# Kernel tuning notes

Hardware: AMD Instinct MI355X
Metric: run time of the kernel (lower is better)

## Reference

```python
import jax, jax.numpy as jnp
import numpy as np

EPS = 1e-12  # F.normalize default eps (denominator = max(norm, eps))


def setup_inputs() -> dict:
    key = jax.random.key(0)
    ks = jax.random.split(key, 8)
    B, FIN, H, W = 4, 256, 64, 64
    N_MEM, SQ = 64, 16           # sqrt_fin = fin**0.5
    POS_CH = 2                    # PosEncoding concatenates one coord channel per dim
    CIN = FIN + POS_CH
    QK = N_MEM * SQ               # 1024
    # PosEncoding buffer: normalized coordinate grid in [-1, 1], shape [2, H, W]
    ys = jnp.linspace(-1.0, 1.0, H, dtype=jnp.float32)
    xs = jnp.linspace(-1.0, 1.0, W, dtype=jnp.float32)
    gy, gx = jnp.meshgrid(ys, xs, indexing='ij')
    pos = jnp.stack([gy, gx], axis=0)
    s = 0.02
    return {
        'x':    jax.random.normal(ks[0], (B, FIN, H, W), jnp.float32),
        'pos':  pos,
        'wq':   jax.random.normal(ks[1], (QK, CIN), jnp.float32) * s,
        'bq':   jnp.zeros((QK,), jnp.float32),
        'wk':   jax.random.normal(ks[2], (QK, CIN), jnp.float32) * s,
        'bk':   jnp.zeros((QK,), jnp.float32),
        'v':    jax.random.normal(ks[3], (N_MEM, FIN), jnp.float32) * s,
        'wout': jax.random.normal(ks[4], (FIN, FIN), jnp.float32) * s,
        'bout': jnp.zeros((FIN,), jnp.float32),
    }


def reference(x, pos, wq, bq, wk, bk, v, wout, bout):
    B, C, H, W = x.shape
    S = H * W
    n_mem, fin = v.shape
    sq = wq.shape[0] // n_mem
    # PosEncoding: concat coordinate channels
    posb = jnp.broadcast_to(pos[None], (B,) + pos.shape)
    xp = jnp.concatenate([x, posb], axis=1).reshape(B, C + pos.shape[0], S)
    # 1x1 conv projections (channel GEMMs)
    q = jnp.einsum('oc,bcs->bos', wq, xp) + bq[None, :, None]  # [B, n_mem*sq, S]
    k = jnp.einsum('oc,bcs->bos', wk, xp) + bk[None, :, None]
    q = q.reshape(B, n_mem, sq, S).transpose(0, 3, 1, 2)  # [B,S,m,sq]
    k = k.reshape(B, n_mem, sq, S).transpose(0, 3, 2, 1)  # [B,S,sq,m]
    # F.normalize: q over last dim (sqrt_fin), k over dim=1 (sqrt_fin)
    qn = q / jnp.maximum(jnp.linalg.norm(q, axis=-1, keepdims=True), EPS)
    kn = k / jnp.maximum(jnp.linalg.norm(k, axis=2, keepdims=True), EPS)
    # attn[b,s,m,n] = qn . kn ; dropout is identity in eval mode.
    # mean over memory slots m commutes with (attn @ v), so fuse:
    attn_mean = jnp.einsum('bsk,bskn->bsn', qn.mean(axis=2), kn)  # [B,S,n_mem]
    mem = attn_mean @ v                                            # [B,S,fin]
    mem = mem.transpose(0, 2, 1).reshape(B, fin, H, W)
    out = jnp.einsum('of,bfhw->bohw', wout, mem) + bout[None, :, None, None]
    return x + out
```

## Files before the change

kernel.cpp:

```cpp
#include <hip/hip_runtime.h>
#include <stdint.h>

#define EPSN 1e-12f

typedef float f32x16 __attribute__((ext_vector_type(16)));
typedef float f32x4 __attribute__((ext_vector_type(4)));
typedef __bf16 bf16x8 __attribute__((ext_vector_type(8)));

__device__ __forceinline__ unsigned short f2bf(float f) {
  union { float f; unsigned int u; } v; v.f = f;
  unsigned int u = v.u + 0x7FFFu + ((v.u >> 16) & 1u);
  return (unsigned short)(u >> 16);
}

#define NKS 17
#define WQF_OFF 0
#define WKF_OFF (32 * NKS * 64 * 8)
#define WVP_OFF (2 * 32 * NKS * 64 * 8)

__global__ __launch_bounds__(256) void prep_kernel(
    const float* __restrict__ wq, const float* __restrict__ bq,
    const float* __restrict__ wk, const float* __restrict__ bk,
    const float* __restrict__ v, const float* __restrict__ wout,
    unsigned short* __restrict__ wsp) {
  int bid = blockIdx.x;
  if (bid < 512) {
    int isK = bid >= 256;
    int ob = (bid & 255) * 4;
    const float* w = isK ? wk : wq;
    const float* bb = isK ? bk : bq;
    unsigned short* dst = wsp + (isK ? WKF_OFF : WQF_OFF);
    for (int i = threadIdx.x; i < 4 * 129; i += 256) {
      int r = i / 129, q = i - r * 129;
      int o = ob + r, k = q * 2;
      float2 w2 = *(const float2*)(w + o * 258 + k);
      int g = o >> 5, col = o & 31;
      int ks = k >> 4, hi = (k >> 3) & 1, j = k & 7;
      uint32_t pk = (uint32_t)f2bf(w2.x) | ((uint32_t)f2bf(w2.y) << 16);
      *(uint32_t*)(dst + (((g * NKS + ks) * 64 + hi * 32 + col) << 3) + j) = pk;
    }
    for (int i = threadIdx.x; i < 4 * 14; i += 256) {
      int r = i / 14, kk = 258 + (i - r * 14);
      int o = ob + r;
      int g = o >> 5, col = o & 31;
      int ks = kk >> 4, hi = (kk >> 3) & 1, j = kk & 7;
      dst[(((g * NKS + ks) * 64 + hi * 32 + col) << 3) + j] =
          (kk == 258) ? f2bf(bb[o]) : (unsigned short)0;
    }
  } else {
    int idx = (bid - 512) * 256 + threadIdx.x;
    int fc = idx & 15, m = (idx >> 4) & 63, o = idx >> 10;
    const f32x4* wo = (const f32x4*)(wout + o * 256 + fc * 16);
    const f32x4* vm = (const f32x4*)(v + m * 256 + fc * 16);
    float s = 0.f;
#pragma unroll
    for (int f = 0; f < 4; ++f) {
      f32x4 a = wo[f], bvv = vm[f];
      s += a[0]*bvv[0] + a[1]*bvv[1] + a[2]*bvv[2] + a[3]*bvv[3];
    }
    s += __shfl_xor(s, 1, 64);
    s += __shfl_xor(s, 2, 64);
    s += __shfl_xor(s, 4, 64);
    s += __shfl_xor(s, 8, 64);
    if (fc == 0) wsp[WVP_OFF + o * 64 + m] = f2bf(s);
  }
}

#define KP 296
#define QS 66
#define AT 72

__global__ __launch_bounds__(1024, 4) void fused_kernel(
    const float* __restrict__ x, const float* __restrict__ pos,
    const unsigned short* __restrict__ wsp, const float* __restrict__ bout,
    float* __restrict__ out) {
  __shared__ __align__(16) unsigned short xp[64 * KP];
  __shared__ __align__(16) float qbarL[16 * QS];
  __shared__ __align__(16) unsigned short attnM[64 * AT];
  __shared__ float boutL[256];

  const int tid = threadIdx.x;
  const int lane = tid & 63;
  const int wid = __builtin_amdgcn_readfirstlane(tid >> 6);
  const int px = lane & 31, q2 = lane >> 5;
  const int P0 = blockIdx.x * 64;
  const int b = P0 >> 12, s0 = P0 & 4095;

  const int wtoff = (2 * wid) * NKS * 512 + lane * 8;
  const unsigned short* wqf = wsp + WQF_OFF + wtoff;
  const unsigned short* wkf = wsp + WKF_OFF + wtoff;

  bf16x8 A0 = *(const bf16x8*)(wqf);
  bf16x8 A1 = *(const bf16x8*)(wqf + NKS * 512);

  uint32_t* xp32 = (uint32_t*)xp;
  {
    const float* xrow = x + b * 256 * 4096 + s0;
    float v0[8], v1[8];
#pragma unroll
    for (int it = 0; it < 8; ++it) {
      int item = tid + it * 1024;
      int pp = item & 63, dcol = item >> 6;
      v0[it] = xrow[(2 * dcol) * 4096 + pp];
      v1[it] = xrow[(2 * dcol + 1) * 4096 + pp];
    }
#pragma unroll
    for (int it = 0; it < 8; ++it) {
      int item = tid + it * 1024;
      int pp = item & 63, dcol = item >> 6;
      xp32[pp * 148 + dcol] =
          (uint32_t)f2bf(v0[it]) | ((uint32_t)f2bf(v1[it]) << 16);
    }
    if (tid < 512) {
      int pp = tid & 63, dcol = 128 + (tid >> 6);
      float t0 = 0.f, t1 = 0.f;
      if (dcol == 128) { t0 = pos[s0 + pp]; t1 = pos[4096 + s0 + pp]; }
      else if (dcol == 129) { t0 = 1.0f; }
      xp32[pp * 148 + dcol] = (uint32_t)f2bf(t0) | ((uint32_t)f2bf(t1) << 16);
    }
  }
  if (tid < 256) boutL[tid] = bout[tid];
  for (int i = tid; i < 16 * QS; i += 1024) qbarL[i] = 0.f;
  __syncthreads();

#define PHASE(WB, AI0, AI1) do {                                          \
    bf16x8 _A0 = (AI0), _A1 = (AI1);                                      \
    _Pragma("unroll")                                                     \
    for (int ks = 0; ks < NKS; ++ks) {                                    \
      bf16x8 _N0 = _A0, _N1 = _A1;                                        \
      if (ks + 1 < NKS) {                                                 \
        _N0 = *(const bf16x8*)((WB) + (ks + 1) * 512);                    \
        _N1 = *(const bf16x8*)((WB) + NKS * 512 + (ks + 1) * 512);        \
      }                                                                   \
      bf16x8 _b0 = *(const bf16x8*)&xp[px * KP + ks * 16 + q2 * 8];       \
      bf16x8 _b1 = *(const bf16x8*)&xp[(32 + px) * KP + ks * 16 + q2 * 8];\
      acc00 = __builtin_amdgcn_mfma_f32_32x32x16_bf16(_A0, _b0, acc00, 0, 0, 0); \
      acc01 = __builtin_amdgcn_mfma_f32_32x32x16_bf16(_A0, _b1, acc01, 0, 0, 0); \
      acc10 = __builtin_amdgcn_mfma_f32_32x32x16_bf16(_A1, _b0, acc10, 0, 0, 0); \
      acc11 = __builtin_amdgcn_mfma_f32_32x32x16_bf16(_A1, _b1, acc11, 0, 0, 0); \
      _A0 = _N0; _A1 = _N1;                                               \
    }                                                                     \
  } while (0)

  f32x16 acc00 = (f32x16)0.f, acc01 = (f32x16)0.f,
         acc10 = (f32x16)0.f, acc11 = (f32x16)0.f;
  PHASE(wqf, A0, A1);

  bf16x8 K0 = *(const bf16x8*)(wkf);
  bf16x8 K1 = *(const bf16x8*)(wkf + NKS * 512);

  {
    float qsum[2][8];
#pragma unroll
    for (int nt = 0; nt < 2; ++nt)
#pragma unroll
      for (int r = 0; r < 8; ++r) qsum[nt][r] = 0.f;
#pragma unroll
    for (int ot = 0; ot < 2; ++ot) {
#pragma unroll
      for (int nt = 0; nt < 2; ++nt) {
        const f32x16 a = ot ? (nt ? acc11 : acc10) : (nt ? acc01 : acc00);
        float s20 = 0.f, s21 = 0.f;
#pragma unroll
        for (int r = 0; r < 8; ++r) {
          s20 = fmaf(a[r], a[r], s20);
          s21 = fmaf(a[r + 8], a[r + 8], s21);
        }
        s20 += __shfl_xor(s20, 32, 64);
        s21 += __shfl_xor(s21, 32, 64);
        float i0 = 1.0f / fmaxf(sqrtf(s20), EPSN);
        float i1 = 1.0f / fmaxf(sqrtf(s21), EPSN);
#pragma unroll
        for (int r = 0; r < 8; ++r) qsum[nt][r] += a[r] * i0 + a[r + 8] * i1;
      }
    }
#pragma unroll
    for (int nt = 0; nt < 2; ++nt)
#pragma unroll
      for (int r = 0; r < 8; ++r) {
        int j = (r & 3) + ((r >> 2) << 3) + (q2 << 2);
        atomicAdd(&qbarL[j * QS + nt * 32 + px], qsum[nt][r] * (1.0f / 64.0f));
      }
  }
  __syncthreads();

  acc00 = (f32x16)0.f; acc01 = (f32x16)0.f;
  acc10 = (f32x16)0.f; acc11 = (f32x16)0.f;
  PHASE(wkf, K0, K1);

  {
    float qb[2][8];
#pragma unroll
    for (int nt = 0; nt < 2; ++nt)
#pragma unroll
      for (int r = 0; r < 8; ++r) {
        int j = (r & 3) + ((r >> 2) << 3) + (q2 << 2);
        qb[nt][r] = qbarL[j * QS + nt * 32 + px];
      }
#pragma unroll
    for (int ot = 0; ot < 2; ++ot) {
#pragma unroll
      for (int nt = 0; nt < 2; ++nt) {
        const f32x16 a = ot ? (nt ? acc11 : acc10) : (nt ? acc01 : acc00);
        float s20 = 0.f, s21 = 0.f, sp0 = 0.f, sp1 = 0.f;
#pragma unroll
        for (int r = 0; r < 8; ++r) {
          s20 = fmaf(a[r], a[r], s20);         sp0 = fmaf(qb[nt][r], a[r], sp0);
          s21 = fmaf(a[r + 8], a[r + 8], s21); sp1 = fmaf(qb[nt][r], a[r + 8], sp1);
        }
        s20 += __shfl_xor(s20, 32, 64);
        s21 += __shfl_xor(s21, 32, 64);
        sp0 += __shfl_xor(sp0, 32, 64);
        sp1 += __shfl_xor(sp1, 32, 64);
        if (q2 == 0) {
          int m0 = wid * 4 + ot * 2;
          attnM[(nt * 32 + px) * AT + m0]     = f2bf(sp0 / fmaxf(sqrtf(s20), EPSN));
          attnM[(nt * 32 + px) * AT + m0 + 1] = f2bf(sp1 / fmaxf(sqrtf(s21), EPSN));
        }
      }
    }
  }
  __syncthreads();

  {
    const int otile = wid >> 1, pxt = wid & 1;
    f32x16 e = (f32x16)0.f;
    const unsigned short* wv = wsp + WVP_OFF + (otile * 32 + px) * 64 + q2 * 8;
    const unsigned short* ab = &attnM[(pxt * 32 + px) * AT + q2 * 8];
#pragma unroll
    for (int ks = 0; ks < 4; ++ks) {
      bf16x8 av = *(const bf16x8*)(wv + ks * 16);
      bf16x8 bv = *(const bf16x8*)(ab + ks * 16);
      e = __builtin_amdgcn_mfma_f32_32x32x16_bf16(av, bv, e, 0, 0, 0);
    }
#pragma unroll
    for (int r = 0; r < 16; ++r) {
      const int o = otile * 32 + (r & 3) + ((r >> 2) << 3) + (q2 << 2);
      const int p = pxt * 32 + px;
      const int gi = (b * 256 + o) * 4096 + s0 + p;
      out[gi] = x[gi] + boutL[o] + e[r];
    }
  }
#undef PHASE
}

extern "C" void kernel_launch(void* const* d_in, const int* in_sizes, int n_in,
                              void* d_out, int out_size, void* d_ws, size_t ws_size,
                              hipStream_t stream) {
  const float* x    = (const float*)d_in[0];
  const float* pos  = (const float*)d_in[1];
  const float* wq   = (const float*)d_in[2];
  const float* bq   = (const float*)d_in[3];
  const float* wk   = (const float*)d_in[4];
  const float* bk   = (const float*)d_in[5];
  const float* v    = (const float*)d_in[6];
  const float* wout = (const float*)d_in[7];
  const float* bout = (const float*)d_in[8];
  float* out = (float*)d_out;
  unsigned short* wsp = (unsigned short*)d_ws;

  hipLaunchKernelGGL(prep_kernel, dim3(1536), dim3(256), 0, stream,
                     wq, bq, wk, bk, v, wout, wsp);
  hipLaunchKernelGGL(fused_kernel, dim3(256), dim3(1024), 0, stream,
                     x, pos, wsp, bout, out);
}
```

Baseline: 134.4 us.

## Halve pixel tile per block to 32 and double grid to 512 blocks

```diff
diff --git a/kernel.cpp b/kernel.cpp
--- a/kernel.cpp
+++ b/kernel.cpp
@@ -66,53 +66,51 @@
   }
 }
 
+#define PXB 32
 #define KP 296
-#define QS 66
-#define AT 72
-
-__global__ __launch_bounds__(1024, 4) void fused_kernel(
+#define QS 34
+#define AT 76
+
+__global__ __launch_bounds__(1024, 8) void fused_kernel(
     const float* __restrict__ x, const float* __restrict__ pos,
     const unsigned short* __restrict__ wsp, const float* __restrict__ bout,
     float* __restrict__ out) {
-  __shared__ __align__(16) unsigned short xp[64 * KP];
+  __shared__ __align__(16) unsigned short xp[PXB * KP];
   __shared__ __align__(16) float qbarL[16 * QS];
-  __shared__ __align__(16) unsigned short attnM[64 * AT];
+  __shared__ __align__(16) unsigned short attnM[PXB * AT];
   __shared__ float boutL[256];
 
   const int tid = threadIdx.x;
   const int lane = tid & 63;
   const int wid = __builtin_amdgcn_readfirstlane(tid >> 6);
   const int px = lane & 31, q2 = lane >> 5;
-  const int P0 = blockIdx.x * 64;
+  const int P0 = blockIdx.x * PXB;
   const int b = P0 >> 12, s0 = P0 & 4095;
 
   const int wtoff = (2 * wid) * NKS * 512 + lane * 8;
   const unsigned short* wqf = wsp + WQF_OFF + wtoff;
   const unsigned short* wkf = wsp + WKF_OFF + wtoff;
 
-  bf16x8 A0 = *(const bf16x8*)(wqf);
-  bf16x8 A1 = *(const bf16x8*)(wqf + NKS * 512);
-
   uint32_t* xp32 = (uint32_t*)xp;
   {
     const float* xrow = x + b * 256 * 4096 + s0;
-    float v0[8], v1[8];
-#pragma unroll
-    for (int it = 0; it < 8; ++it) {
+    float v0[4], v1[4];
+#pragma unroll
+    for (int it = 0; it < 4; ++it) {
       int item = tid + it * 1024;
-      int pp = item & 63, dcol = item >> 6;
+      int pp = item & 31, dcol = item >> 5;
       v0[it] = xrow[(2 * dcol) * 4096 + pp];
       v1[it] = xrow[(2 * dcol + 1) * 4096 + pp];
     }
 #pragma unroll
-    for (int it = 0; it < 8; ++it) {
+    for (int it = 0; it < 4; ++it) {
       int item = tid + it * 1024;
-      int pp = item & 63, dcol = item >> 6;
+      int pp = item & 31, dcol = item >> 5;
       xp32[pp * 148 + dcol] =
           (uint32_t)f2bf(v0[it]) | ((uint32_t)f2bf(v1[it]) << 16);
     }
-    if (tid < 512) {
-      int pp = tid & 63, dcol = 128 + (tid >> 6);
+    if (tid < 256) {
+      int pp = tid & 31, dcol = 128 + (tid >> 5);
       float t0 = 0.f, t1 = 0.f;
       if (dcol == 128) { t0 = pos[s0 + pp]; t1 = pos[4096 + s0 + pp]; }
       else if (dcol == 129) { t0 = 1.0f; }
@@ -123,110 +121,85 @@
   for (int i = tid; i < 16 * QS; i += 1024) qbarL[i] = 0.f;
   __syncthreads();
 
-#define PHASE(WB, AI0, AI1) do {                                          \
-    bf16x8 _A0 = (AI0), _A1 = (AI1);                                      \
+#define PHASE(WB) do {                                                    \
     _Pragma("unroll")                                                     \
     for (int ks = 0; ks < NKS; ++ks) {                                    \
-      bf16x8 _N0 = _A0, _N1 = _A1;                                        \
-      if (ks + 1 < NKS) {                                                 \
-        _N0 = *(const bf16x8*)((WB) + (ks + 1) * 512);                    \
-        _N1 = *(const bf16x8*)((WB) + NKS * 512 + (ks + 1) * 512);        \
-      }                                                                   \
+      bf16x8 _A0 = *(const bf16x8*)((WB) + ks * 512);                     \
+      bf16x8 _A1 = *(const bf16x8*)((WB) + NKS * 512 + ks * 512);         \
       bf16x8 _b0 = *(const bf16x8*)&xp[px * KP + ks * 16 + q2 * 8];       \
-      bf16x8 _b1 = *(const bf16x8*)&xp[(32 + px) * KP + ks * 16 + q2 * 8];\
-      acc00 = __builtin_amdgcn_mfma_f32_32x32x16_bf16(_A0, _b0, acc00, 0, 0, 0); \
-      acc01 = __builtin_amdgcn_mfma_f32_32x32x16_bf16(_A0, _b1, acc01, 0, 0, 0); \
-      acc10 = __builtin_amdgcn_mfma_f32_32x32x16_bf16(_A1, _b0, acc10, 0, 0, 0); \
-      acc11 = __builtin_amdgcn_mfma_f32_32x32x16_bf16(_A1, _b1, acc11, 0, 0, 0); \
-      _A0 = _N0; _A1 = _N1;                                               \
+      acc0 = __builtin_amdgcn_mfma_f32_32x32x16_bf16(_A0, _b0, acc0, 0, 0, 0); \
+      acc1 = __builtin_amdgcn_mfma_f32_32x32x16_bf16(_A1, _b0, acc1, 0, 0, 0); \
     }                                                                     \
   } while (0)
 
-  f32x16 acc00 = (f32x16)0.f, acc01 = (f32x16)0.f,
-         acc10 = (f32x16)0.f, acc11 = (f32x16)0.f;
-  PHASE(wqf, A0, A1);
-
-  bf16x8 K0 = *(const bf16x8*)(wkf);
-  bf16x8 K1 = *(const bf16x8*)(wkf + NKS * 512);
+  f32x16 acc0 = (f32x16)0.f, acc1 = (f32x16)0.f;
+  PHASE(wqf);
 
   {
-    float qsum[2][8];
-#pragma unroll
-    for (int nt = 0; nt < 2; ++nt)
-#pragma unroll
-      for (int r = 0; r < 8; ++r) qsum[nt][r] = 0.f;
+    float qsum[8];
+#pragma unroll
+    for (int r = 0; r < 8; ++r) qsum[r] = 0.f;
 #pragma unroll
     for (int ot = 0; ot < 2; ++ot) {
-#pragma unroll
-      for (int nt = 0; nt < 2; ++nt) {
-        const f32x16 a = ot ? (nt ? acc11 : acc10) : (nt ? acc01 : acc00);
-        float s20 = 0.f, s21 = 0.f;
-#pragma unroll
-        for (int r = 0; r < 8; ++r) {
-          s20 = fmaf(a[r], a[r], s20);
-          s21 = fmaf(a[r + 8], a[r + 8], s21);
-        }
-        s20 += __shfl_xor(s20, 32, 64);
-        s21 += __shfl_xor(s21, 32, 64);
-        float i0 = 1.0f / fmaxf(sqrtf(s20), EPSN);
-        float i1 = 1.0f / fmaxf(sqrtf(s21), EPSN);
-#pragma unroll
-        for (int r = 0; r < 8; ++r) qsum[nt][r] += a[r] * i0 + a[r + 8] * i1;
+      const f32x16 a = ot ? acc1 : acc0;
+      float s20 = 0.f, s21 = 0.f;
+#pragma unroll
+      for (int r = 0; r < 8; ++r) {
+        s20 = fmaf(a[r], a[r], s20);
+        s21 = fmaf(a[r + 8], a[r + 8], s21);
       }
-    }
-#pragma unroll
-    for (int nt = 0; nt < 2; ++nt)
+      s20 += __shfl_xor(s20, 32, 64);
+      s21 += __shfl_xor(s21, 32, 64);
+      float i0 = 1.0f / fmaxf(sqrtf(s20), EPSN);
+      float i1 = 1.0f / fmaxf(sqrtf(s21), EPSN);
+#pragma unroll
+      for (int r = 0; r < 8; ++r) qsum[r] += a[r] * i0 + a[r + 8] * i1;
+    }
+#pragma unroll
+    for (int r = 0; r < 8; ++r) {
+      int j = (r & 3) + ((r >> 2) << 3) + (q2 << 2);
+      atomicAdd(&qbarL[j * QS + px], qsum[r] * (1.0f / 64.0f));
+    }
+  }
+
+  acc0 = (f32x16)0.f; acc1 = (f32x16)0.f;
+  PHASE(wkf);
+  __syncthreads();
+
+  {
+    float qb[8];
+#pragma unroll
+    for (int r = 0; r < 8; ++r) {
+      int j = (r & 3) + ((r >> 2) << 3) + (q2 << 2);
+      qb[r] = qbarL[j * QS + px];
+    }
+#pragma unroll
+    for (int ot = 0; ot < 2; ++ot) {
+      const f32x16 a = ot ? acc1 : acc0;
+      float s20 = 0.f, s21 = 0.f, sp0 = 0.f, sp1 = 0.f;
 #pragma unroll
       for (int r = 0; r < 8; ++r) {
-        int j = (r & 3) + ((r >> 2) << 3) + (q2 << 2);
-        atomicAdd(&qbarL[j * QS + nt * 32 + px], qsum[nt][r] * (1.0f / 64.0f));
+        s20 = fmaf(a[r], a[r], s20);         sp0 = fmaf(qb[r], a[r], sp0);
+        s21 = fmaf(a[r + 8], a[r + 8], s21); sp1 = fmaf(qb[r], a[r + 8], sp1);
       }
+      s20 += __shfl_xor(s20, 32, 64);
+      s21 += __shfl_xor(s21, 32, 64);
+      sp0 += __shfl_xor(sp0, 32, 64);
+      sp1 += __shfl_xor(sp1, 32, 64);
+      if (q2 == 0) {
+        int m0 = wid * 4 + ot * 2;
+        attnM[px * AT + m0]     = f2bf(sp0 / fmaxf(sqrtf(s20), EPSN));
+        attnM[px * AT + m0 + 1] = f2bf(sp1 / fmaxf(sqrtf(s21), EPSN));
+      }
+    }
   }
   __syncthreads();
 
-  acc00 = (f32x16)0.f; acc01 = (f32x16)0.f;
-  acc10 = (f32x16)0.f; acc11 = (f32x16)0.f;
-  PHASE(wkf, K0, K1);
-
-  {
-    float qb[2][8];
-#pragma unroll
-    for (int nt = 0; nt < 2; ++nt)
-#pragma unroll
-      for (int r = 0; r < 8; ++r) {
-        int j = (r & 3) + ((r >> 2) << 3) + (q2 << 2);
-        qb[nt][r] = qbarL[j * QS + nt * 32 + px];
-      }
-#pragma unroll
-    for (int ot = 0; ot < 2; ++ot) {
-#pragma unroll
-      for (int nt = 0; nt < 2; ++nt) {
-        const f32x16 a = ot ? (nt ? acc11 : acc10) : (nt ? acc01 : acc00);
-        float s20 = 0.f, s21 = 0.f, sp0 = 0.f, sp1 = 0.f;
-#pragma unroll
-        for (int r = 0; r < 8; ++r) {
-          s20 = fmaf(a[r], a[r], s20);         sp0 = fmaf(qb[nt][r], a[r], sp0);
-          s21 = fmaf(a[r + 8], a[r + 8], s21); sp1 = fmaf(qb[nt][r], a[r + 8], sp1);
-        }
-        s20 += __shfl_xor(s20, 32, 64);
-        s21 += __shfl_xor(s21, 32, 64);
-        sp0 += __shfl_xor(sp0, 32, 64);
-        sp1 += __shfl_xor(sp1, 32, 64);
-        if (q2 == 0) {
-          int m0 = wid * 4 + ot * 2;
-          attnM[(nt * 32 + px) * AT + m0]     = f2bf(sp0 / fmaxf(sqrtf(s20), EPSN));
-          attnM[(nt * 32 + px) * AT + m0 + 1] = f2bf(sp1 / fmaxf(sqrtf(s21), EPSN));
-        }
-      }
-    }
-  }
-  __syncthreads();
-
-  {
-    const int otile = wid >> 1, pxt = wid & 1;
+  if (wid < 8) {
+    const int otile = wid;
     f32x16 e = (f32x16)0.f;
     const unsigned short* wv = wsp + WVP_OFF + (otile * 32 + px) * 64 + q2 * 8;
-    const unsigned short* ab = &attnM[(pxt * 32 + px) * AT + q2 * 8];
+    const unsigned short* ab = &attnM[px * AT + q2 * 8];
 #pragma unroll
     for (int ks = 0; ks < 4; ++ks) {
       bf16x8 av = *(const bf16x8*)(wv + ks * 16);
@@ -236,8 +209,7 @@
 #pragma unroll
     for (int r = 0; r < 16; ++r) {
       const int o = otile * 32 + (r & 3) + ((r >> 2) << 3) + (q2 << 2);
-      const int p = pxt * 32 + px;
-      const int gi = (b * 256 + o) * 4096 + s0 + p;
+      const int gi = (b * 256 + o) * 4096 + s0 + px;
       out[gi] = x[gi] + boutL[o] + e[r];
     }
   }
@@ -261,6 +233,6 @@
 
   hipLaunchKernelGGL(prep_kernel, dim3(1536), dim3(256), 0, stream,
                      wq, bq, wk, bk, v, wout, wsp);
-  hipLaunchKernelGGL(fused_kernel, dim3(256), dim3(1024), 0, stream,
+  hipLaunchKernelGGL(fused_kernel, dim3(512), dim3(1024), 0, stream,
                      x, pos, wsp, bout, out);
 }
```

New measurement: 128.4 us. 4.5% less time.

## Rotate weight tile assignment per block, deepen weight prefetch, move barrier after K GEMM

Applied to the files above, without the earlier changes.

```diff
diff --git a/kernel.cpp b/kernel.cpp
--- a/kernel.cpp
+++ b/kernel.cpp
@@ -66,6 +66,7 @@
   }
 }
 
+#define PXB 64
 #define KP 296
 #define QS 66
 #define AT 72
@@ -74,24 +75,26 @@
     const float* __restrict__ x, const float* __restrict__ pos,
     const unsigned short* __restrict__ wsp, const float* __restrict__ bout,
     float* __restrict__ out) {
-  __shared__ __align__(16) unsigned short xp[64 * KP];
+  __shared__ __align__(16) unsigned short xp[PXB * KP];
   __shared__ __align__(16) float qbarL[16 * QS];
-  __shared__ __align__(16) unsigned short attnM[64 * AT];
+  __shared__ __align__(16) unsigned short attnM[PXB * AT];
   __shared__ float boutL[256];
 
   const int tid = threadIdx.x;
   const int lane = tid & 63;
   const int wid = __builtin_amdgcn_readfirstlane(tid >> 6);
   const int px = lane & 31, q2 = lane >> 5;
-  const int P0 = blockIdx.x * 64;
+  const int bid = blockIdx.x;
+  const int P0 = bid * PXB;
   const int b = P0 >> 12, s0 = P0 & 4095;
 
-  const int wtoff = (2 * wid) * NKS * 512 + lane * 8;
-  const unsigned short* wqf = wsp + WQF_OFF + wtoff;
-  const unsigned short* wkf = wsp + WKF_OFF + wtoff;
-
-  bf16x8 A0 = *(const bf16x8*)(wqf);
-  bf16x8 A1 = *(const bf16x8*)(wqf + NKS * 512);
+  const int rot2 = (bid & 15) << 1;
+  const int ti0 = (2 * wid + rot2) & 31;
+  const int ti1 = ti0 + 1;
+  const unsigned short* wq0 = wsp + WQF_OFF + ti0 * (NKS * 512) + lane * 8;
+  const unsigned short* wq1 = wsp + WQF_OFF + ti1 * (NKS * 512) + lane * 8;
+  const unsigned short* wk0 = wsp + WKF_OFF + ti0 * (NKS * 512) + lane * 8;
+  const unsigned short* wk1 = wsp + WKF_OFF + ti1 * (NKS * 512) + lane * 8;
 
   uint32_t* xp32 = (uint32_t*)xp;
   {
@@ -123,14 +126,18 @@
   for (int i = tid; i < 16 * QS; i += 1024) qbarL[i] = 0.f;
   __syncthreads();
 
-#define PHASE(WB, AI0, AI1) do {                                          \
-    bf16x8 _A0 = (AI0), _A1 = (AI1);                                      \
+#define PHASE(W0, W1) do {                                                \
+    bf16x8 ra0[2], ra1[2];                                                \
+    ra0[0] = *(const bf16x8*)((W0));                                      \
+    ra1[0] = *(const bf16x8*)((W1));                                      \
+    ra0[1] = *(const bf16x8*)((W0) + 512);                                \
+    ra1[1] = *(const bf16x8*)((W1) + 512);                                \
     _Pragma("unroll")                                                     \
     for (int ks = 0; ks < NKS; ++ks) {                                    \
-      bf16x8 _N0 = _A0, _N1 = _A1;                                        \
-      if (ks + 1 < NKS) {                                                 \
-        _N0 = *(const bf16x8*)((WB) + (ks + 1) * 512);                    \
-        _N1 = *(const bf16x8*)((WB) + NKS * 512 + (ks + 1) * 512);        \
+      bf16x8 _A0 = ra0[ks & 1], _A1 = ra1[ks & 1];                        \
+      if (ks + 2 < NKS) {                                                 \
+        ra0[ks & 1] = *(const bf16x8*)((W0) + (ks + 2) * 512);            \
+        ra1[ks & 1] = *(const bf16x8*)((W1) + (ks + 2) * 512);            \
       }                                                                   \
       bf16x8 _b0 = *(const bf16x8*)&xp[px * KP + ks * 16 + q2 * 8];       \
       bf16x8 _b1 = *(const bf16x8*)&xp[(32 + px) * KP + ks * 16 + q2 * 8];\
@@ -138,16 +145,12 @@
       acc01 = __builtin_amdgcn_mfma_f32_32x32x16_bf16(_A0, _b1, acc01, 0, 0, 0); \
       acc10 = __builtin_amdgcn_mfma_f32_32x32x16_bf16(_A1, _b0, acc10, 0, 0, 0); \
       acc11 = __builtin_amdgcn_mfma_f32_32x32x16_bf16(_A1, _b1, acc11, 0, 0, 0); \
-      _A0 = _N0; _A1 = _N1;                                               \
     }                                                                     \
   } while (0)
 
   f32x16 acc00 = (f32x16)0.f, acc01 = (f32x16)0.f,
          acc10 = (f32x16)0.f, acc11 = (f32x16)0.f;
-  PHASE(wqf, A0, A1);
-
-  bf16x8 K0 = *(const bf16x8*)(wkf);
-  bf16x8 K1 = *(const bf16x8*)(wkf + NKS * 512);
+  PHASE(wq0, wq1);
 
   {
     float qsum[2][8];
@@ -182,11 +185,11 @@
         atomicAdd(&qbarL[j * QS + nt * 32 + px], qsum[nt][r] * (1.0f / 64.0f));
       }
   }
-  __syncthreads();
 
   acc00 = (f32x16)0.f; acc01 = (f32x16)0.f;
   acc10 = (f32x16)0.f; acc11 = (f32x16)0.f;
-  PHASE(wkf, K0, K1);
+  PHASE(wk0, wk1);
+  __syncthreads();
 
   {
     float qb[2][8];
@@ -199,6 +202,7 @@
       }
 #pragma unroll
     for (int ot = 0; ot < 2; ++ot) {
+      const int m0 = (ot ? ti1 : ti0) * 2;
 #pragma unroll
       for (int nt = 0; nt < 2; ++nt) {
         const f32x16 a = ot ? (nt ? acc11 : acc10) : (nt ? acc01 : acc00);
@@ -213,7 +217,6 @@
         sp0 += __shfl_xor(sp0, 32, 64);
         sp1 += __shfl_xor(sp1, 32, 64);
         if (q2 == 0) {
-          int m0 = wid * 4 + ot * 2;
           attnM[(nt * 32 + px) * AT + m0]     = f2bf(sp0 / fmaxf(sqrtf(s20), EPSN));
           attnM[(nt * 32 + px) * AT + m0 + 1] = f2bf(sp1 / fmaxf(sqrtf(s21), EPSN));
         }
```

Result: faster. 129.0 us (-4.0%).
